# Kernel tuning notes

Hardware: AMD Instinct MI355X
Metric: run time of the kernel (lower is better)

The kernel has to match this reference:

```python
import jax, jax.numpy as jnp
import numpy as np

# Static config (init_kwargs)
H = 56; W = 56; C = 256; NH = 8; WS = 7; SS = 3
HD = C // NH
SCALE = HD ** -0.5
N = WS * WS                      # tokens per window = 49
NW = (H // WS) * (W // WS)       # windows per image = 64
HIDDEN = int(C * 4.0)
EPS = 1e-5


def _rel_pos_index():
    coords = np.stack(np.meshgrid(np.arange(WS), np.arange(WS), indexing='ij')).reshape(2, -1)
    rel = coords[:, :, None] - coords[:, None, :]          # [2, N, N]
    rel = rel.transpose(1, 2, 0).astype(np.int64)          # [N, N, 2]
    rel[:, :, 0] += WS - 1
    rel[:, :, 1] += WS - 1
    rel[:, :, 0] *= 2 * WS - 1
    return rel.sum(-1).reshape(-1)                         # [N*N]


def _attn_mask():
    # (0 / -100) mask for the shifted-window configuration, [NW, N, N]
    img = np.zeros([H, W])
    cnt = 0
    for hs in (slice(0, -WS), slice(-WS, -SS), slice(-SS, None)):
        for ws in (slice(0, -WS), slice(-WS, -SS), slice(-SS, None)):
            img[hs, ws] = cnt
            cnt += 1
    mw = img.reshape(H // WS, WS, W // WS, WS).transpose(0, 2, 1, 3).reshape(-1, N)
    diff = mw[:, None, :] - mw[:, :, None]                 # [NW, N, N]
    return np.where(diff != 0, -100.0, 0.0).astype(np.float32)


_REL_IDX = _rel_pos_index()
_MASK = _attn_mask()


def _ln(x, g, b):
    mu = jnp.mean(x, axis=-1, keepdims=True)
    var = jnp.mean((x - mu) ** 2, axis=-1, keepdims=True)
    return (x - mu) * jax.lax.rsqrt(var + EPS) * g + b


def setup_inputs() -> dict:
    key = jax.random.key(0)
    ks = jax.random.split(key, 16)
    B = 32
    s = 0.02
    return {
        'x': jax.random.normal(ks[0], (B, H * W, C), dtype=jnp.float32),
        'gamma1': jnp.ones((C,), jnp.float32),
        'beta1': jnp.zeros((C,), jnp.float32),
        'qkv_w': jax.random.normal(ks[1], (C, 3 * C), jnp.float32) * s,
        'qkv_b': jnp.zeros((3 * C,), jnp.float32),
        'proj_w': jax.random.normal(ks[2], (C, C), jnp.float32) * s,
        'proj_b': jnp.zeros((C,), jnp.float32),
        'rpb_table': jax.random.normal(ks[3], ((2 * WS - 1) * (2 * WS - 1), NH), jnp.float32) * s,
        'gamma2': jnp.ones((C,), jnp.float32),
        'beta2': jnp.zeros((C,), jnp.float32),
        'fc1_w': jax.random.normal(ks[4], (C, HIDDEN), jnp.float32) * s,
        'fc1_b': jnp.zeros((HIDDEN,), jnp.float32),
        'fc2_w': jax.random.normal(ks[5], (HIDDEN, C), jnp.float32) * s,
        'fc2_b': jnp.zeros((C,), jnp.float32),
    }


def reference(x, gamma1, beta1, qkv_w, qkv_b, proj_w, proj_b, rpb_table,
              gamma2, beta2, fc1_w, fc1_b, fc2_w, fc2_b):
    B = x.shape[0]
    y = _ln(x, gamma1, beta1).reshape(B, H, W, C)
    # cyclic shift
    y = jnp.roll(y, (-SS, -SS), axis=(1, 2))
    # window partition -> [B*NW, N, C]
    win = y.reshape(B, H // WS, WS, W // WS, WS, C)
    win = win.transpose(0, 1, 3, 2, 4, 5).reshape(-1, N, C)
    # qkv projection, split heads
    qkv = (win @ qkv_w + qkv_b).reshape(-1, N, 3, NH, HD).transpose(2, 0, 3, 1, 4)
    q, k, v = qkv[0] * SCALE, qkv[1], qkv[2]            # [B*NW, NH, N, HD]
    attn = jnp.einsum('bhnd,bhmd->bhnm', q, k)          # [B*NW, NH, N, N]
    # gathered relative position bias
    bias = rpb_table[jnp.asarray(_REL_IDX)].reshape(N, N, NH).transpose(2, 0, 1)
    attn = attn + bias[None]
    # shift mask
    mask = jnp.asarray(_MASK)                           # [NW, N, N]
    attn = attn.reshape(B, NW, NH, N, N) + mask[None, :, None]
    attn = jax.nn.softmax(attn.reshape(-1, NH, N, N), axis=-1)
    o = jnp.einsum('bhnm,bhmd->bnhd', attn, v).reshape(-1, N, C)
    o = o @ proj_w + proj_b
    # window reverse + reverse shift
    o = o.reshape(B, H // WS, W // WS, WS, WS, C).transpose(0, 1, 3, 2, 4, 5).reshape(B, H, W, C)
    o = jnp.roll(o, (SS, SS), axis=(1, 2)).reshape(B, H * W, C)
    x = x + o
    # MLP block
    y = _ln(x, gamma2, beta2)
    y = jax.nn.gelu(y @ fc1_w + fc1_b, approximate=False) @ fc2_w + fc2_b
    return x + y
```

## Files before the change

kernel.cpp:

```cpp
#include <hip/hip_runtime.h>
#include <hip/hip_bf16.h>
#include <math.h>


typedef __bf16 bf16_t;
typedef __bf16 bf16x4 __attribute__((ext_vector_type(4)));
typedef __bf16 bf16x8 __attribute__((ext_vector_type(8)));
typedef float f32x4 __attribute__((ext_vector_type(4)));

#define AS1 __attribute__((address_space(1)))
#define AS3 __attribute__((address_space(3)))

__device__ __forceinline__ void gload_lds16(const bf16_t* g, bf16_t* l) {
  __builtin_amdgcn_global_load_lds((AS1 void*)g, (AS3 void*)l, 16, 0, 0);
}

__global__ void transpose_cast3(const float* __restrict__ qkv_w,
                                const float* __restrict__ proj_w,
                                const float* __restrict__ fc1_w,
                                bf16_t* __restrict__ qkvWt,
                                bf16_t* __restrict__ projWt,
                                bf16_t* __restrict__ fc1Wt) {
  int idx = blockIdx.x * 256 + threadIdx.x;
  const float* w;
  bf16_t* wt;
  int N;
  if (blockIdx.y == 0) { w = qkv_w; wt = qkvWt; N = 768; }
  else if (blockIdx.y == 1) { w = proj_w; wt = projWt; N = 256; }
  else { w = fc1_w; wt = fc1Wt; N = 1024; }
  if (idx < N * 256) {
    int n = idx >> 8, k = idx & 255;
    wt[idx] = (bf16_t)w[(size_t)k * N + n];
  }
}

__global__ void transpose_cast(const float* __restrict__ w, bf16_t* __restrict__ wt,
                               int K, int N) {
  int idx = blockIdx.x * 256 + threadIdx.x;
  if (idx < N * K) {
    int n = idx / K, k = idx - n * K;
    wt[idx] = (bf16_t)w[(size_t)k * N + n];
  }
}

__global__ void build_bm(const float* __restrict__ rpb, float* __restrict__ bm) {
  int t = blockIdx.x, h = blockIdx.y;
  int wr = (t & 2) ? 7 : 0, wc = (t & 1) ? 7 : 0;
  for (int e = threadIdx.x; e < 4096; e += 256) {
    int r = e >> 6, c = e & 63;
    float v;
    if (c >= 49) {
      v = -30000.f;
    } else if (r >= 49) {
      v = 0.f;
    } else {
      int r1 = r / 7, c1 = r - r1 * 7;
      int r2 = c / 7, c2 = c - r2 * 7;
      v = rpb[((r1 - r2 + 6) * 13 + (c1 - c2 + 6)) * 8 + h];
      int hp = wr * 7 + r1, wp = wc * 7 + c1;
      int hq = wr * 7 + r2, wq = wc * 7 + c2;
      int ri = (hp < 49 ? 0 : (hp < 53 ? 1 : 2)) * 3 + (wp < 49 ? 0 : (wp < 53 ? 1 : 2));
      int rj = (hq < 49 ? 0 : (hq < 53 ? 1 : 2)) * 3 + (wq < 49 ? 0 : (wq < 53 ? 1 : 2));
      if (ri != rj) v -= 100.f;
    }
    bm[((size_t)(t * 8 + h) * 64 + r) * 64 + c] = v;
  }
}

__global__ __launch_bounds__(256)
void ln_cast(const float* __restrict__ src, const float* __restrict__ gamma,
             const float* __restrict__ beta, bf16_t* __restrict__ dst, int windowed) {
  int row = blockIdx.x * 4 + (threadIdx.x >> 6);
  int lane = threadIdx.x & 63;
  size_t srow;
  if (windowed) {
    int w = row / 49, t = row - w * 49;
    int img = w >> 6, wi = w & 63;
    int wr = wi >> 3, wc = wi & 7;
    int rr = t / 7, cc = t - rr * 7;
    int h = wr * 7 + rr + 3; if (h >= 56) h -= 56;
    int ww = wc * 7 + cc + 3; if (ww >= 56) ww -= 56;
    srow = (size_t)img * 3136 + h * 56 + ww;
  } else {
    srow = row;
  }
  float4 v = *(const float4*)(src + srow * 256 + lane * 4);
  float s = v.x + v.y + v.z + v.w;
  float s2 = v.x * v.x + v.y * v.y + v.z * v.z + v.w * v.w;
#pragma unroll
  for (int off = 32; off > 0; off >>= 1) {
    s += __shfl_xor(s, off);
    s2 += __shfl_xor(s2, off);
  }
  float mu = s * (1.0f / 256.0f);
  float rs = rsqrtf(s2 * (1.0f / 256.0f) - mu * mu + 1e-5f);
  float4 g = *(const float4*)(gamma + lane * 4);
  float4 b = *(const float4*)(beta + lane * 4);
  bf16x4 o;
  o[0] = (bf16_t)((v.x - mu) * rs * g.x + b.x);
  o[1] = (bf16_t)((v.y - mu) * rs * g.y + b.y);
  o[2] = (bf16_t)((v.z - mu) * rs * g.z + b.z);
  o[3] = (bf16_t)((v.w - mu) * rs * g.w + b.w);
  *(bf16x4*)(dst + (size_t)row * 256 + lane * 4) = o;
}

template <int MODE>
__global__ __launch_bounds__(256)
void gemm_bt(const bf16_t* __restrict__ A, const bf16_t* __restrict__ Bt,
             const float* __restrict__ bias,
             bf16_t* Cbf, float* Cf, const float* Res,
             int M, int N, int K, int nblk) {
  __shared__ __align__(16) bf16_t As[128 * 32];
  __shared__ __align__(16) bf16_t Bs[128 * 32];
  const int tid = threadIdx.x;
  const int lane = tid & 63;
  const int wave = tid >> 6;
  const int wm = wave & 1, wn = wave >> 1;
  const int bid = blockIdx.x;
  const int m_idx = bid / nblk;
  const int n_idx = bid - m_idx * nblk;
  const int m0 = m_idx * 128;
  const int n0 = n_idx * 128;

  f32x4 acc[4][4];
#pragma unroll
  for (int i = 0; i < 4; i++)
#pragma unroll
    for (int j = 0; j < 4; j++) acc[i][j] = f32x4{0.f, 0.f, 0.f, 0.f};

  const bf16_t* Ag = A + (size_t)m0 * K;
  const bf16_t* Bg = Bt + (size_t)n0 * K;
  const int lr = lane & 15;
  const int kq = (lane >> 4) * 8;

  for (int k0 = 0; k0 < K; k0 += 32) {
#pragma unroll
    for (int it = 0; it < 2; it++) {
      int slot = it * 256 + tid;
      int row = slot >> 2;
      int ko = (slot & 3) << 3;
      bf16_t* ldsA = As + (it * 256 + wave * 64) * 8;
      bf16_t* ldsB = Bs + (it * 256 + wave * 64) * 8;
      gload_lds16(Ag + (size_t)row * K + k0 + ko, ldsA);
      gload_lds16(Bg + (size_t)row * K + k0 + ko, ldsB);
    }
    __syncthreads();
    bf16x8 af[4], bfr[4];
#pragma unroll
    for (int i = 0; i < 4; i++) {
      af[i]  = *(const bf16x8*)(As + (wm * 64 + i * 16 + lr) * 32 + kq);
      bfr[i] = *(const bf16x8*)(Bs + (wn * 64 + i * 16 + lr) * 32 + kq);
    }
#pragma unroll
    for (int i = 0; i < 4; i++)
#pragma unroll
      for (int j = 0; j < 4; j++)
        acc[i][j] = __builtin_amdgcn_mfma_f32_16x16x32_bf16(af[i], bfr[j], acc[i][j], 0, 0, 0);
    __syncthreads();
  }

  const int quad = lane >> 4;
#pragma unroll
  for (int i = 0; i < 4; i++) {
    int rbase = m0 + wm * 64 + i * 16 + quad * 4;
#pragma unroll
    for (int j = 0; j < 4; j++) {
      int col = n0 + wn * 64 + j * 16 + lr;
      float bi = bias[col];
#pragma unroll
      for (int r = 0; r < 4; r++) {
        int row = rbase + r;
        float v = acc[i][j][r] + bi;
        if (MODE == 0) {
          Cbf[(size_t)row * N + col] = (bf16_t)v;
        } else {
          int w = row / 49, t = row - w * 49;
          int img = w >> 6, wi = w & 63;
          int wr = wi >> 3, wc = wi & 7;
          int rr = t / 7, cc = t - rr * 7;
          int h = wr * 7 + rr + 3; if (h >= 56) h -= 56;
          int ww2 = wc * 7 + cc + 3; if (ww2 >= 56) ww2 -= 56;
          size_t idx = ((size_t)img * 3136 + h * 56 + ww2) * 256 + col;
          Cf[idx] = v + Res[idx];
        }
      }
    }
  }
}

__global__ __launch_bounds__(256)
void attn_mfma(const bf16_t* __restrict__ qkv, const float* __restrict__ bm,
               bf16_t* __restrict__ o) {
  __shared__ __align__(16) bf16_t Ps[64 * 72];
  __shared__ __align__(16) bf16_t Vt[32 * 72];
  const int w = blockIdx.x, h = blockIdx.y;
  const int tid = threadIdx.x;
  const int lane = tid & 63, wv = tid >> 6;
  const int lr = lane & 15, quad = lane >> 4;
  const int wi = w & 63;
  const int mtype = (((wi >> 3) == 7) ? 2 : 0) | (((wi & 7) == 7) ? 1 : 0);
  const bf16_t* base = qkv + (size_t)w * 49 * 768 + h * 32;

  bf16x8 zero8;
#pragma unroll
  for (int z = 0; z < 8; z++) zero8[z] = (bf16_t)0.f;

  {
    int tok = tid >> 2, d8 = (tid & 3) * 8;
    bf16x8 v8 = zero8;
    if (tok < 49) v8 = *(const bf16x8*)(base + (size_t)tok * 768 + 512 + d8);
#pragma unroll
    for (int z = 0; z < 8; z++) Vt[(d8 + z) * 72 + tok] = v8[z];
  }
  __syncthreads();

  const int mrow = 16 * wv + lr;
  bf16x8 aq = zero8;
  if (mrow < 49) aq = *(const bf16x8*)(base + (size_t)mrow * 768 + quad * 8);
  f32x4 s[4];
#pragma unroll
  for (int j = 0; j < 4; j++) {
    int nrow = 16 * j + lr;
    bf16x8 bk = zero8;
    if (nrow < 49) bk = *(const bf16x8*)(base + (size_t)nrow * 768 + 256 + quad * 8);
    s[j] = __builtin_amdgcn_mfma_f32_16x16x32_bf16(aq, bk, f32x4{0.f, 0.f, 0.f, 0.f}, 0, 0, 0);
  }

  const float* bmb = bm + ((size_t)(mtype * 8 + h) * 64 + 16 * wv) * 64;
  float inv[4];
#pragma unroll
  for (int reg = 0; reg < 4; reg++) {
    int rl = quad * 4 + reg;
    float v0[4];
    float mx = -1e30f;
#pragma unroll
    for (int j = 0; j < 4; j++) {
      float v = s[j][reg] * 0.17677669529663689f + bmb[rl * 64 + 16 * j + lr];
      v0[j] = v;
      mx = fmaxf(mx, v);
    }
#pragma unroll
    for (int off = 8; off > 0; off >>= 1) mx = fmaxf(mx, __shfl_xor(mx, off));
    float sum = 0.f;
#pragma unroll
    for (int j = 0; j < 4; j++) {
      float e = __expf(v0[j] - mx);
      v0[j] = e;
      sum += e;
    }
#pragma unroll
    for (int off = 8; off > 0; off >>= 1) sum += __shfl_xor(sum, off);
    inv[reg] = 1.0f / sum;
#pragma unroll
    for (int j = 0; j < 4; j++)
      Ps[(16 * wv + rl) * 72 + 16 * j + lr] = (bf16_t)v0[j];
  }

  f32x4 oacc[2];
  oacc[0] = f32x4{0.f, 0.f, 0.f, 0.f};
  oacc[1] = f32x4{0.f, 0.f, 0.f, 0.f};
#pragma unroll
  for (int kk = 0; kk < 2; kk++) {
    bf16x8 ap = *(const bf16x8*)(Ps + (16 * wv + lr) * 72 + kk * 32 + quad * 8);
#pragma unroll
    for (int n = 0; n < 2; n++) {
      bf16x8 bv = *(const bf16x8*)(Vt + (16 * n + lr) * 72 + kk * 32 + quad * 8);
      oacc[n] = __builtin_amdgcn_mfma_f32_16x16x32_bf16(ap, bv, oacc[n], 0, 0, 0);
    }
  }
#pragma unroll
  for (int n = 0; n < 2; n++) {
#pragma unroll
    for (int reg = 0; reg < 4; reg++) {
      int row = 16 * wv + quad * 4 + reg;
      if (row < 49) {
        int d = 16 * n + lr;
        o[((size_t)w * 49 + row) * 256 + h * 32 + d] = (bf16_t)(oacc[n][reg] * inv[reg]);
      }
    }
  }
}

__global__ __launch_bounds__(256, 3)
void fused_mlp(const bf16_t* __restrict__ y2, const bf16_t* __restrict__ W1t,
               const float* __restrict__ b1, const bf16_t* __restrict__ W2t,
               const float* __restrict__ b2, float* __restrict__ out) {
  __shared__ __align__(16) bf16_t Ws[8192];
  __shared__ __align__(16) bf16_t Hs[64 * 136];
  const int tid = threadIdx.x;
  const int lane = tid & 63, wave = tid >> 6;
  const int lr = lane & 15, quad = lane >> 4;
  const int wr = wave & 1, wc = wave >> 1;
  const int m0 = blockIdx.x * 64;
  const bf16_t* Arow0 = y2 + (size_t)(m0 + 32 * wr + lr) * 256;
  const bf16_t* Arow1 = y2 + (size_t)(m0 + 32 * wr + 16 + lr) * 256;

  f32x4 acc2[2][8];
#pragma unroll
  for (int i = 0; i < 2; i++)
#pragma unroll
    for (int n = 0; n < 8; n++) acc2[i][n] = f32x4{0.f, 0.f, 0.f, 0.f};

  for (int hc = 0; hc < 8; hc++) {
    f32x4 acc1[2][4];
#pragma unroll
    for (int i = 0; i < 2; i++)
#pragma unroll
      for (int j = 0; j < 4; j++) acc1[i][j] = f32x4{0.f, 0.f, 0.f, 0.f};

    for (int ks = 0; ks < 4; ks++) {
      __syncthreads();
#pragma unroll
      for (int r = 0; r < 4; r++) {
        int sub = r >> 1, half = r & 1;
        int row = half * 64 + (tid >> 2), k8 = tid & 3;
        const bf16_t* src = W1t + (size_t)(hc * 128 + row) * 256 + ks * 64 + sub * 32 + k8 * 8;
        gload_lds16(src, Ws + sub * 4096 + half * 2048 + wave * 512);
      }
      bf16x8 a[2][2];
#pragma unroll
      for (int kk = 0; kk < 2; kk++) {
        a[kk][0] = *(const bf16x8*)(Arow0 + ks * 64 + kk * 32 + quad * 8);
        a[kk][1] = *(const bf16x8*)(Arow1 + ks * 64 + kk * 32 + quad * 8);
      }
      __syncthreads();
#pragma unroll
      for (int kk = 0; kk < 2; kk++) {
        bf16x8 b[4];
#pragma unroll
        for (int j = 0; j < 4; j++)
          b[j] = *(const bf16x8*)(Ws + kk * 4096 + (64 * wc + 16 * j + lr) * 32 + quad * 8);
#pragma unroll
        for (int i = 0; i < 2; i++)
#pragma unroll
          for (int j = 0; j < 4; j++)
            acc1[i][j] = __builtin_amdgcn_mfma_f32_16x16x32_bf16(a[kk][i], b[j], acc1[i][j], 0, 0, 0);
      }
    }
#pragma unroll
    for (int i = 0; i < 2; i++) {
#pragma unroll
      for (int j = 0; j < 4; j++) {
        float bias1 = b1[hc * 128 + 64 * wc + 16 * j + lr];
        int hcol = 64 * wc + 16 * j + lr;
#pragma unroll
        for (int reg = 0; reg < 4; reg++) {
          int row_l = 32 * wr + 16 * i + quad * 4 + reg;
          float v = acc1[i][j][reg] + bias1;
          float arg = fminf(v * (0.7978845608f + 0.0356774081f * v * v), 15.f);
          float e = __expf(2.f * arg);
          float g = v * (e / (e + 1.f));
          Hs[row_l * 136 + hcol] = (bf16_t)g;
        }
      }
    }
    for (int ks2 = 0; ks2 < 4; ks2++) {
      __syncthreads();
#pragma unroll
      for (int r = 0; r < 4; r++) {
        int row = r * 64 + (tid >> 2), k8 = tid & 3;
        const bf16_t* src = W2t + (size_t)row * 1024 + hc * 128 + ks2 * 32 + k8 * 8;
        gload_lds16(src, Ws + r * 2048 + wave * 512);
      }
      __syncthreads();
      bf16x8 ah[2], bw[8];
#pragma unroll
      for (int i = 0; i < 2; i++)
        ah[i] = *(const bf16x8*)(Hs + (32 * wr + 16 * i + lr) * 136 + ks2 * 32 + quad * 8);
#pragma unroll
      for (int n = 0; n < 8; n++)
        bw[n] = *(const bf16x8*)(Ws + (128 * wc + 16 * n + lr) * 32 + quad * 8);
#pragma unroll
      for (int i = 0; i < 2; i++)
#pragma unroll
        for (int n = 0; n < 8; n++)
          acc2[i][n] = __builtin_amdgcn_mfma_f32_16x16x32_bf16(ah[i], bw[n], acc2[i][n], 0, 0, 0);
    }
  }

#pragma unroll
  for (int i = 0; i < 2; i++) {
#pragma unroll
    for (int n = 0; n < 8; n++) {
      int col = 128 * wc + 16 * n + lr;
      float bi = b2[col];
#pragma unroll
      for (int reg = 0; reg < 4; reg++) {
        int row = m0 + 32 * wr + 16 * i + quad * 4 + reg;
        size_t idx = (size_t)row * 256 + col;
        out[idx] = acc2[i][n][reg] + bi + out[idx];
      }
    }
  }
}

extern "C" void kernel_launch(void* const* d_in, const int* in_sizes, int n_in,
                              void* d_out, int out_size, void* d_ws, size_t ws_size,
                              hipStream_t stream) {
  const float* x      = (const float*)d_in[0];
  const float* g1     = (const float*)d_in[1];
  const float* b1     = (const float*)d_in[2];
  const float* qkv_w  = (const float*)d_in[3];
  const float* qkv_b  = (const float*)d_in[4];
  const float* proj_w = (const float*)d_in[5];
  const float* proj_b = (const float*)d_in[6];
  const float* rpb    = (const float*)d_in[7];
  const float* g2     = (const float*)d_in[8];
  const float* b2     = (const float*)d_in[9];
  const float* fc1_w  = (const float*)d_in[10];
  const float* fc1_b  = (const float*)d_in[11];
  const float* fc2_w  = (const float*)d_in[12];
  const float* fc2_b  = (const float*)d_in[13];
  float* out = (float*)d_out;
  char* ws = (char*)d_ws;

  bf16_t* xw   = (bf16_t*)ws;
  bf16_t* qkv  = (bf16_t*)(ws + 51380224);
  bf16_t* ow   = (bf16_t*)(ws + 205520896);
  bf16_t* y2   = xw;
  bf16_t* qkvWt  = (bf16_t*)(ws + 256901120);
  bf16_t* projWt = qkvWt + 768 * 256;
  bf16_t* fc1Wt  = projWt + 256 * 256;
  bf16_t* fc2Wt  = fc1Wt + 1024 * 256;
  float*  bm     = (float*)fc2Wt;

  transpose_cast3<<<dim3(1024, 3), 256, 0, stream>>>(qkv_w, proj_w, fc1_w,
                                                     qkvWt, projWt, fc1Wt);
  build_bm<<<dim3(4, 8), 256, 0, stream>>>(rpb, bm);

  ln_cast<<<25088, 256, 0, stream>>>(x, g1, b1, xw, 1);
  gemm_bt<0><<<784 * 6, 256, 0, stream>>>(xw, qkvWt, qkv_b, qkv, nullptr, nullptr,
                                          100352, 768, 256, 6);
  attn_mfma<<<dim3(2048, 8), 256, 0, stream>>>(qkv, bm, ow);
  transpose_cast<<<(256 * 1024 + 255) / 256, 256, 0, stream>>>(fc2_w, fc2Wt, 1024, 256);
  gemm_bt<3><<<784 * 2, 256, 0, stream>>>(ow, projWt, proj_b, nullptr, out, x,
                                          100352, 256, 256, 2);
  ln_cast<<<25088, 256, 0, stream>>>(out, g2, b2, y2, 0);
  fused_mlp<<<1568, 256, 0, stream>>>(y2, fc1Wt, fc1_b, fc2Wt, fc2_b, out);
}
```

Measured before the change: 828.9 us.

## Restructure fused MLP: per-wave row tiles, register-resident A, exact erf GELU

Re-partitions the fused MLP block so each wave owns 16 full rows instead of a 2x2 row/column split. The activation rows for the whole K dimension are held in registers and reused across all hidden chunks, so they are loaded once. Weight tiles are staged in LDS in larger K steps (128 for fc1, 64 for fc2), which halves the number of barrier-separated stages. The hidden tile becomes per-wave, and the tanh-style GELU is replaced by exact erf GELU. In exchange, each wave now issues more LDS weight reads per MFMA, uses more registers and LDS (which may lower occupancy), and erf costs more than the approximation.

New measurement: 767.7 us. 7.4% less time.

```diff
diff --git a/kernel.cpp b/kernel.cpp
--- a/kernel.cpp
+++ b/kernel.cpp
@@ -285,111 +285,99 @@
 void fused_mlp(const bf16_t* __restrict__ y2, const bf16_t* __restrict__ W1t,
                const float* __restrict__ b1, const bf16_t* __restrict__ W2t,
                const float* __restrict__ b2, float* __restrict__ out) {
-  __shared__ __align__(16) bf16_t Ws[8192];
-  __shared__ __align__(16) bf16_t Hs[64 * 136];
+  __shared__ __align__(16) bf16_t Ws[16384];
+  __shared__ __align__(16) bf16_t Hs[4 * 16 * 136];
   const int tid = threadIdx.x;
   const int lane = tid & 63, wave = tid >> 6;
   const int lr = lane & 15, quad = lane >> 4;
-  const int wr = wave & 1, wc = wave >> 1;
   const int m0 = blockIdx.x * 64;
-  const bf16_t* Arow0 = y2 + (size_t)(m0 + 32 * wr + lr) * 256;
-  const bf16_t* Arow1 = y2 + (size_t)(m0 + 32 * wr + 16 + lr) * 256;
-
-  f32x4 acc2[2][8];
-#pragma unroll
-  for (int i = 0; i < 2; i++)
-#pragma unroll
-    for (int n = 0; n < 8; n++) acc2[i][n] = f32x4{0.f, 0.f, 0.f, 0.f};
+  bf16_t* HsW = Hs + wave * (16 * 136);
+
+  const bf16_t* Arow = y2 + (size_t)(m0 + 16 * wave + lr) * 256;
+  bf16x8 aF[2][4];
+#pragma unroll
+  for (int ks = 0; ks < 2; ks++)
+#pragma unroll
+    for (int kk = 0; kk < 4; kk++)
+      aF[ks][kk] = *(const bf16x8*)(Arow + ks * 128 + kk * 32 + quad * 8);
+
+  f32x4 acc2[16];
+#pragma unroll
+  for (int n = 0; n < 16; n++) acc2[n] = f32x4{0.f, 0.f, 0.f, 0.f};
 
   for (int hc = 0; hc < 8; hc++) {
-    f32x4 acc1[2][4];
-#pragma unroll
-    for (int i = 0; i < 2; i++)
-#pragma unroll
-      for (int j = 0; j < 4; j++) acc1[i][j] = f32x4{0.f, 0.f, 0.f, 0.f};
-
-    for (int ks = 0; ks < 4; ks++) {
+    f32x4 acc1[8];
+#pragma unroll
+    for (int j = 0; j < 8; j++) acc1[j] = f32x4{0.f, 0.f, 0.f, 0.f};
+
+    for (int ks = 0; ks < 2; ks++) {
       __syncthreads();
 #pragma unroll
-      for (int r = 0; r < 4; r++) {
-        int sub = r >> 1, half = r & 1;
-        int row = half * 64 + (tid >> 2), k8 = tid & 3;
-        const bf16_t* src = W1t + (size_t)(hc * 128 + row) * 256 + ks * 64 + sub * 32 + k8 * 8;
-        gload_lds16(src, Ws + sub * 4096 + half * 2048 + wave * 512);
-      }
-      bf16x8 a[2][2];
+      for (int kk = 0; kk < 4; kk++) {
+#pragma unroll
+        for (int it = 0; it < 2; it++) {
+          int row = it * 64 + wave * 16 + (lane >> 2);
+          int k8 = lane & 3;
+          const bf16_t* src = W1t + (size_t)(hc * 128 + row) * 256
+                              + ks * 128 + kk * 32 + k8 * 8;
+          gload_lds16(src, Ws + kk * 4096 + (it * 64 + wave * 16) * 32);
+        }
+      }
+      __syncthreads();
+#pragma unroll
+      for (int kk = 0; kk < 4; kk++) {
+#pragma unroll
+        for (int j = 0; j < 8; j++) {
+          bf16x8 b = *(const bf16x8*)(Ws + kk * 4096 + (16 * j + lr) * 32 + quad * 8);
+          acc1[j] = __builtin_amdgcn_mfma_f32_16x16x32_bf16(aF[ks][kk], b, acc1[j], 0, 0, 0);
+        }
+      }
+    }
+#pragma unroll
+    for (int j = 0; j < 8; j++) {
+      float bias1 = b1[hc * 128 + 16 * j + lr];
+#pragma unroll
+      for (int reg = 0; reg < 4; reg++) {
+        float v = acc1[j][reg] + bias1;
+        v = 0.5f * v * (1.0f + erff(v * 0.70710678118654752f));
+        HsW[(4 * quad + reg) * 136 + 16 * j + lr] = (bf16_t)v;
+      }
+    }
+    for (int ks2 = 0; ks2 < 2; ks2++) {
+      __syncthreads();
 #pragma unroll
       for (int kk = 0; kk < 2; kk++) {
-        a[kk][0] = *(const bf16x8*)(Arow0 + ks * 64 + kk * 32 + quad * 8);
-        a[kk][1] = *(const bf16x8*)(Arow1 + ks * 64 + kk * 32 + quad * 8);
+#pragma unroll
+        for (int it = 0; it < 4; it++) {
+          int row = it * 64 + wave * 16 + (lane >> 2);
+          int k8 = lane & 3;
+          const bf16_t* src = W2t + (size_t)row * 1024
+                              + hc * 128 + ks2 * 64 + kk * 32 + k8 * 8;
+          gload_lds16(src, Ws + kk * 8192 + (it * 64 + wave * 16) * 32);
+        }
       }
       __syncthreads();
 #pragma unroll
       for (int kk = 0; kk < 2; kk++) {
-        bf16x8 b[4];
-#pragma unroll
-        for (int j = 0; j < 4; j++)
-          b[j] = *(const bf16x8*)(Ws + kk * 4096 + (64 * wc + 16 * j + lr) * 32 + quad * 8);
-#pragma unroll
-        for (int i = 0; i < 2; i++)
-#pragma unroll
-          for (int j = 0; j < 4; j++)
-            acc1[i][j] = __builtin_amdgcn_mfma_f32_16x16x32_bf16(a[kk][i], b[j], acc1[i][j], 0, 0, 0);
-      }
-    }
-#pragma unroll
-    for (int i = 0; i < 2; i++) {
-#pragma unroll
-      for (int j = 0; j < 4; j++) {
-        float bias1 = b1[hc * 128 + 64 * wc + 16 * j + lr];
-        int hcol = 64 * wc + 16 * j + lr;
-#pragma unroll
-        for (int reg = 0; reg < 4; reg++) {
-          int row_l = 32 * wr + 16 * i + quad * 4 + reg;
-          float v = acc1[i][j][reg] + bias1;
-          float arg = fminf(v * (0.7978845608f + 0.0356774081f * v * v), 15.f);
-          float e = __expf(2.f * arg);
-          float g = v * (e / (e + 1.f));
-          Hs[row_l * 136 + hcol] = (bf16_t)g;
+        bf16x8 ah = *(const bf16x8*)(HsW + lr * 136 + ks2 * 64 + kk * 32 + quad * 8);
+#pragma unroll
+        for (int n = 0; n < 16; n++) {
+          bf16x8 bw = *(const bf16x8*)(Ws + kk * 8192 + (16 * n + lr) * 32 + quad * 8);
+          acc2[n] = __builtin_amdgcn_mfma_f32_16x16x32_bf16(ah, bw, acc2[n], 0, 0, 0);
         }
       }
     }
-    for (int ks2 = 0; ks2 < 4; ks2++) {
-      __syncthreads();
-#pragma unroll
-      for (int r = 0; r < 4; r++) {
-        int row = r * 64 + (tid >> 2), k8 = tid & 3;
-        const bf16_t* src = W2t + (size_t)row * 1024 + hc * 128 + ks2 * 32 + k8 * 8;
-        gload_lds16(src, Ws + r * 2048 + wave * 512);
-      }
-      __syncthreads();
-      bf16x8 ah[2], bw[8];
-#pragma unroll
-      for (int i = 0; i < 2; i++)
-        ah[i] = *(const bf16x8*)(Hs + (32 * wr + 16 * i + lr) * 136 + ks2 * 32 + quad * 8);
-#pragma unroll
-      for (int n = 0; n < 8; n++)
-        bw[n] = *(const bf16x8*)(Ws + (128 * wc + 16 * n + lr) * 32 + quad * 8);
-#pragma unroll
-      for (int i = 0; i < 2; i++)
-#pragma unroll
-        for (int n = 0; n < 8; n++)
-          acc2[i][n] = __builtin_amdgcn_mfma_f32_16x16x32_bf16(ah[i], bw[n], acc2[i][n], 0, 0, 0);
-    }
-  }
-
-#pragma unroll
-  for (int i = 0; i < 2; i++) {
-#pragma unroll
-    for (int n = 0; n < 8; n++) {
-      int col = 128 * wc + 16 * n + lr;
-      float bi = b2[col];
-#pragma unroll
-      for (int reg = 0; reg < 4; reg++) {
-        int row = m0 + 32 * wr + 16 * i + quad * 4 + reg;
-        size_t idx = (size_t)row * 256 + col;
-        out[idx] = acc2[i][n][reg] + bi + out[idx];
-      }
+  }
+
+#pragma unroll
+  for (int n = 0; n < 16; n++) {
+    int col = 16 * n + lr;
+    float bi = b2[col];
+#pragma unroll
+    for (int reg = 0; reg < 4; reg++) {
+      int row = m0 + 16 * wave + 4 * quad + reg;
+      size_t idx = (size_t)row * 256 + col;
+      out[idx] = acc2[n][reg] + bi + out[idx];
     }
   }
 }
```
